# Kernel tuning notes

Hardware: AMD Instinct MI355X
Metric: run time of the kernel (lower is better)

## Reference

```python
import jax, jax.numpy as jnp
import numpy as np

EMBED = 512
WINDOW = 64

def setup_inputs() -> dict:
    key = jax.random.key(0)
    ks = jax.random.split(key, 5)
    B, S, E = 4, 4096, EMBED
    s = 1.0 / np.sqrt(E)
    x = jax.random.normal(ks[0], (B, S, E), dtype=jnp.float32)
    W_qkv = jax.random.uniform(ks[1], (E, 3 * E), minval=-s, maxval=s, dtype=jnp.float32)
    b_qkv = jax.random.uniform(ks[2], (3 * E,), minval=-s, maxval=s, dtype=jnp.float32)
    W_out = jax.random.uniform(ks[3], (E, E), minval=-s, maxval=s, dtype=jnp.float32)
    b_out = jax.random.uniform(ks[4], (E,), minval=-s, maxval=s, dtype=jnp.float32)
    return {"x": x, "W_qkv": W_qkv, "b_qkv": b_qkv, "W_out": W_out, "b_out": b_out}

def reference(x, W_qkv, b_qkv, W_out, b_out):
    B, S, E = x.shape
    scale = jnp.sqrt(jnp.asarray(E, dtype=x.dtype))
    qkv = x @ W_qkv + b_qkv                    # [B,S,3E]
    q, k, v = jnp.split(qkv, 3, axis=-1)       # each [B,S,E]
    scores = jnp.einsum('bqe,bke->bqk', q, k) / scale  # [B,S,S]
    pos = jnp.arange(S)
    dist = pos[None, :] - pos[:, None]         # [S,S]
    window_mask = jnp.abs(dist) <= WINDOW
    neg_inf = jnp.asarray(-jnp.inf, dtype=scores.dtype)
    scores = jnp.where(window_mask[None, :, :], scores, neg_inf)
    attn = jax.nn.softmax(scores, axis=-1)     # every row has in-window entries
    attended = jnp.einsum('bqk,bke->bqe', attn, v)
    return attended @ W_out + b_out
```

## Files before the change

### kernel.cpp

```cpp
#include <hip/hip_runtime.h>

typedef __attribute__((ext_vector_type(8))) _Float16 f16x8;
typedef __attribute__((ext_vector_type(4))) _Float16 f16x4;
typedef __attribute__((ext_vector_type(4))) float f32x4;
typedef __attribute__((address_space(1))) const char gc_char;
typedef __attribute__((address_space(3))) char ls_char;

#define MFMA(a, b, c) __builtin_amdgcn_mfma_f32_16x16x32_f16((a), (b), (c), 0, 0, 0)
#define FENCE() asm volatile("" ::: "memory")
#define BARRIER() do { FENCE(); __builtin_amdgcn_s_barrier(); FENCE(); } while (0)
#define VMW(n) asm volatile("s_waitcnt vmcnt(" #n ")" ::: "memory")

static constexpr int SEQ = 4096;
static constexpr int EMB = 512;
static constexpr float QSCALE = 0.04419417382415922f;

__device__ __forceinline__ void gl_lds16(const void* g, void* l) {
    __builtin_amdgcn_global_load_lds((gc_char*)g, (ls_char*)l, 16, 0, 0);
}

__global__ void k_prep(const float* __restrict__ x, _Float16* __restrict__ xb,
                       const float* __restrict__ Wq, _Float16* __restrict__ WqT,
                       const float* __restrict__ Wo, _Float16* __restrict__ WoT) {
    const int bid = blockIdx.x, tid = threadIdx.x;
    if (bid < 4096) {
        long i = (long)bid * 256 + tid;
        const float4* p = (const float4*)x + i * 2;
        float4 a = p[0], b = p[1];
        f16x8 v;
        v[0] = (_Float16)a.x; v[1] = (_Float16)a.y; v[2] = (_Float16)a.z; v[3] = (_Float16)a.w;
        v[4] = (_Float16)b.x; v[5] = (_Float16)b.y; v[6] = (_Float16)b.z; v[7] = (_Float16)b.w;
        *(f16x8*)(xb + i * 8) = v;
    } else {
        __shared__ float Ls[64][65];
        int t = bid - 4096;
        const float* W; _Float16* WT; int N, k0, n0;
        if (t < 192) { W = Wq; WT = WqT; N = 1536; k0 = (t & 7) * 64; n0 = (t >> 3) * 64; }
        else { t -= 192; W = Wo; WT = WoT; N = 512; k0 = (t & 7) * 64; n0 = (t >> 3) * 64; }
        int c = tid & 63, r4 = tid >> 6;
#pragma unroll
        for (int i = 0; i < 16; ++i) {
            int row = i * 4 + r4;
            Ls[row][c] = W[(long)(k0 + row) * N + n0 + c];
        }
        __syncthreads();
#pragma unroll
        for (int i = 0; i < 16; ++i) {
            int row = i * 4 + r4;
            WT[(long)(n0 + row) * 512 + k0 + c] = (_Float16)Ls[c][row];
        }
    }
}

__launch_bounds__(512, 1) __global__
void k_gemm_qkv(const _Float16* __restrict__ A, const _Float16* __restrict__ BT,
                const float* __restrict__ bias,
                _Float16* __restrict__ Qo, _Float16* __restrict__ Ko, _Float16* __restrict__ VT) {
    extern __shared__ __align__(16) char smem[];
    const int tid = threadIdx.x, lane = tid & 63, w = tid >> 6, g = lane >> 4, f = lane & 15;
    const int wrow = w >> 2, wcol = w & 3;
    const int bid = blockIdx.x;
    const int swz = (bid & 7) * 96 + (bid >> 3);
    const int brow = swz / 6, bcol = swz - brow * 6;
    const long row0 = (long)brow * 128;
    const int col0 = bcol * 256;
    const char* Abase = (const char*)A + row0 * 1024;
    const char* Bbase = (const char*)BT + (long)col0 * 1024;

    f32x4 acc[4][4] = {};
    f16x8 a[2][2], breg[2][2][2];

    auto stageA = [&](int h, char* dst, int kt) {
        int rr = tid >> 3;
        int ch = (tid & 7) ^ (rr & 7);
        int grow = h * 32 + (rr & 31) + (rr >> 5) * 64;
        gl_lds16(Abase + (long)grow * 1024 + kt * 128 + ch * 16, dst + h * 8192 + tid * 16);
    };
    auto stageB = [&](int h, char* dst, int kt) {
#pragma unroll
        for (int it = 0; it < 2; ++it) {
            int s = it * 512 + tid;
            int cc = s >> 3;
            int ch = (s & 7) ^ (cc & 7);
            int gcol = h * 32 + (cc & 31) + (cc >> 5) * 64;
            gl_lds16(Bbase + (long)gcol * 1024 + kt * 128 + ch * 16,
                     dst + 16384 + h * 16384 + s * 16);
        }
    };
    auto ldA = [&](const char* buf, int mh) {
#pragma unroll
        for (int mi = 0; mi < 2; ++mi)
#pragma unroll
            for (int ks = 0; ks < 2; ++ks) {
                int rr = wrow * 32 + mi * 16 + f;
                int cl = ks * 4 + g;
                a[mi][ks] = *(const f16x8*)(buf + mh * 8192 + rr * 128 + ((cl ^ (rr & 7)) << 4));
            }
    };
    auto ldB = [&](const char* buf, int nh) {
#pragma unroll
        for (int ni = 0; ni < 2; ++ni)
#pragma unroll
            for (int ks = 0; ks < 2; ++ks) {
                int cc = wcol * 32 + ni * 16 + f;
                int cl = ks * 4 + g;
                breg[nh][ni][ks] =
                    *(const f16x8*)(buf + 16384 + nh * 16384 + cc * 128 + ((cl ^ (cc & 7)) << 4));
            }
    };
    auto mfma8 = [&](int mh, int nh) {
        __builtin_amdgcn_s_setprio(1);
#pragma unroll
        for (int mi = 0; mi < 2; ++mi)
#pragma unroll
            for (int ni = 0; ni < 2; ++ni)
#pragma unroll
                for (int ks = 0; ks < 2; ++ks)
                    acc[mh * 2 + mi][nh * 2 + ni] =
                        MFMA(a[mi][ks], breg[nh][ni][ks], acc[mh * 2 + mi][nh * 2 + ni]);
        __builtin_amdgcn_s_setprio(0);
    };

    stageB(0, smem, 0);
    stageA(0, smem, 0); stageA(1, smem, 0);
    stageB(1, smem, 0);
    VMW(3);
    BARRIER();

    for (int kt = 0; kt < 8; ++kt) {
        const char* cur = smem + (kt & 1) * 49152;
        char* nxt = smem + ((kt + 1) & 1) * 49152;
        const bool last = (kt == 7);
        ldA(cur, 0); ldB(cur, 0);
        if (!last) stageB(0, nxt, kt + 1);
        BARRIER();
        mfma8(0, 0);
        if (!last) { VMW(2); } else { VMW(0); }
        BARRIER();
        ldB(cur, 1);
        if (!last) { stageA(0, nxt, kt + 1); stageA(1, nxt, kt + 1); }
        BARRIER();
        mfma8(0, 1);
        BARRIER();
        ldA(cur, 1);
        if (!last) stageB(1, nxt, kt + 1);
        BARRIER();
        mfma8(1, 0);
        BARRIER();
        mfma8(1, 1);
        if (!last) { VMW(3); }
        BARRIER();
    }

    float bv[4];
#pragma unroll
    for (int ni = 0; ni < 4; ++ni) bv[ni] = bias[col0 + wcol * 64 + ni * 16 + f];

    if (col0 >= 1024) {
#pragma unroll
        for (int mi = 0; mi < 4; ++mi)
#pragma unroll
            for (int ni = 0; ni < 4; ++ni) {
                int r0 = wrow * 64 + mi * 16 + g * 4;
                int c = wcol * 64 + ni * 16 + f;
                f16x4 v4;
#pragma unroll
                for (int j = 0; j < 4; ++j) v4[j] = (_Float16)(acc[mi][ni][j] + bv[ni]);
                *(f16x4*)(smem + c * 256 + ((r0 * 2) ^ ((c & 7) << 4))) = v4;
            }
        __syncthreads();
        int bb = (int)(row0 >> 12);
        _Float16* vt = VT + ((long)bb * 512 + (col0 - 1024)) * 4096 + (row0 & 4095);
#pragma unroll
        for (int it = 0; it < 8; ++it) {
            int slot = it * 512 + tid;
            int e = slot >> 4, ch = slot & 15;
            f16x8 v = *(const f16x8*)(smem + e * 256 + ((ch * 16) ^ ((e & 7) << 4)));
            *(f16x8*)(vt + (long)e * 4096 + ch * 8) = v;
        }
    } else {
        const float sc = (col0 < 512) ? QSCALE : 1.0f;
#pragma unroll
        for (int mi = 0; mi < 4; ++mi)
#pragma unroll
            for (int ni = 0; ni < 4; ++ni)
#pragma unroll
                for (int j = 0; j < 4; ++j) {
                    int r = wrow * 64 + mi * 16 + g * 4 + j;
                    int c = wcol * 64 + ni * 16 + f;
                    float v = (acc[mi][ni][j] + bv[ni]) * sc;
                    int pc = ((c >> 3) + ((r >> 2) & 7) * 2) & 31;
                    *(_Float16*)(smem + r * 512 + pc * 16 + (c & 7) * 2) = (_Float16)v;
                }
        __syncthreads();
        _Float16* dst = (col0 < 512) ? Qo : Ko;
        int cofs = (col0 < 512) ? col0 : col0 - 512;
#pragma unroll
        for (int it = 0; it < 8; ++it) {
            int slot = it * 512 + tid;
            int r = slot >> 5, ch = slot & 31;
            int pc = (ch + ((r >> 2) & 7) * 2) & 31;
            f16x8 v = *(const f16x8*)(smem + r * 512 + pc * 16);
            *(f16x8*)(dst + (row0 + r) * 512 + cofs + ch * 8) = v;
        }
    }
}

__launch_bounds__(512, 1) __global__
void k_attn(const _Float16* __restrict__ Qb, const _Float16* __restrict__ Kb,
            const _Float16* __restrict__ VT, const _Float16* __restrict__ WoT,
            const float* __restrict__ bout, float* __restrict__ Out) {
    extern __shared__ __align__(16) char smem[];
    char* buf[2] = { smem, smem + 49152 };
    char* Pl = smem + 98304;
    float* Mp = (float*)(smem + 123904);
    float* Lp = (float*)(smem + 124928);

    const int tid = threadIdx.x, w = tid >> 6, lane = tid & 63, g = lane >> 4, f = lane & 15;
    const int rh = w >> 2, kh = w & 3;
    const int bid = blockIdx.x;
    const int swzb = (bid & 7) * 32 + (bid >> 3);
    const int b = swzb >> 6, qt = swzb & 63;
    const int q0 = qt * 64, kbase = q0 - 64;
    const long bofs = (long)b * SEQ;

    f16x8 qf[2][16];
#pragma unroll
    for (int mt = 0; mt < 2; ++mt) {
        const _Float16* qr = Qb + (bofs + q0 + rh * 32 + mt * 16 + f) * EMB + g * 8;
#pragma unroll
        for (int ks = 0; ks < 16; ++ks) qf[mt][ks] = *(const f16x8*)(qr + ks * 32);
    }

    auto stageK = [&](int ec, char* dst) {
#pragma unroll
        for (int it = 0; it < 6; ++it) {
            int slot = it * 512 + tid;
            int r = slot >> 4, c = slot & 15;
            int cs = c ^ (r & 7);
            int key = min(max(kbase + r, 0), SEQ - 1);
            gl_lds16(Kb + (bofs + key) * EMB + ec * 128 + cs * 8, dst + slot * 16);
        }
    };
    auto stageVT = [&](int ec, char* dst) {
#pragma unroll
        for (int it = 0; it < 6; ++it) {
            int slot = it * 512 + tid;
            int r = slot / 24, c = slot - r * 24;
            int cs = c ^ (r & 7);
            int k0 = min(max(kbase + cs * 8, 0), SEQ - 8);
            gl_lds16(VT + ((long)b * 512 + ec * 128 + r) * 4096 + k0, dst + slot * 16);
        }
    };

    f32x4 sacc[2][3] = {};
    stageK(0, buf[0]);
    for (int ec = 0; ec < 4; ++ec) {
        if (ec < 3) stageK(ec + 1, buf[(ec + 1) & 1]);
        else stageVT(0, buf[0]);
        VMW(6);
        BARRIER();
        const char* kb = buf[ec & 1];
#pragma unroll
        for (int kk = 0; kk < 4; ++kk) {
#pragma unroll
            for (int t = 0; t < 3; ++t) {
                int n = kh * 48 + t * 16 + f;
                f16x8 bf = *(const f16x8*)(kb + n * 256 + (((kk * 4 + g) ^ (n & 7)) << 4));
#pragma unroll
                for (int mt = 0; mt < 2; ++mt)
                    sacc[mt][t] = MFMA(qf[mt][ec * 4 + kk], bf, sacc[mt][t]);
            }
        }
        BARRIER();
    }

    float m[2][4] = {{-3e30f, -3e30f, -3e30f, -3e30f}, {-3e30f, -3e30f, -3e30f, -3e30f}};
    float l[2][4] = {};
#pragma unroll
    for (int mt = 0; mt < 2; ++mt)
#pragma unroll
        for (int t = 0; t < 3; ++t) {
            int key = kbase + kh * 48 + t * 16 + f;
            bool kv = (key >= 0) && (key < SEQ);
#pragma unroll
            for (int j = 0; j < 4; ++j) {
                int d = key - (q0 + rh * 32 + mt * 16 + g * 4 + j);
                bool valid = kv && (d >= -64) && (d <= 64);
                float s = valid ? sacc[mt][t][j] : -3e30f;
                sacc[mt][t][j] = s;
                m[mt][j] = fmaxf(m[mt][j], s);
            }
        }
#pragma unroll
    for (int mt = 0; mt < 2; ++mt)
#pragma unroll
        for (int j = 0; j < 4; ++j) {
            m[mt][j] = fmaxf(m[mt][j], __shfl_xor(m[mt][j], 1));
            m[mt][j] = fmaxf(m[mt][j], __shfl_xor(m[mt][j], 2));
            m[mt][j] = fmaxf(m[mt][j], __shfl_xor(m[mt][j], 4));
            m[mt][j] = fmaxf(m[mt][j], __shfl_xor(m[mt][j], 8));
        }
    if (f == 0) {
#pragma unroll
        for (int mt = 0; mt < 2; ++mt)
#pragma unroll
            for (int j = 0; j < 4; ++j)
                Mp[kh * 64 + rh * 32 + mt * 16 + g * 4 + j] = m[mt][j];
    }
    __syncthreads();
#pragma unroll
    for (int mt = 0; mt < 2; ++mt)
#pragma unroll
        for (int j = 0; j < 4; ++j) {
            int r = rh * 32 + mt * 16 + g * 4 + j;
            m[mt][j] = fmaxf(fmaxf(Mp[r], Mp[64 + r]), fmaxf(Mp[128 + r], Mp[192 + r]));
        }
#pragma unroll
    for (int mt = 0; mt < 2; ++mt)
#pragma unroll
        for (int t = 0; t < 3; ++t)
#pragma unroll
            for (int j = 0; j < 4; ++j) {
                float p = __expf(sacc[mt][t][j] - m[mt][j]);
                sacc[mt][t][j] = p;
                l[mt][j] += p;
            }
#pragma unroll
    for (int mt = 0; mt < 2; ++mt)
#pragma unroll
        for (int j = 0; j < 4; ++j) {
            l[mt][j] += __shfl_xor(l[mt][j], 1);
            l[mt][j] += __shfl_xor(l[mt][j], 2);
            l[mt][j] += __shfl_xor(l[mt][j], 4);
            l[mt][j] += __shfl_xor(l[mt][j], 8);
        }
    if (f == 0) {
#pragma unroll
        for (int mt = 0; mt < 2; ++mt)
#pragma unroll
            for (int j = 0; j < 4; ++j)
                Lp[kh * 64 + rh * 32 + mt * 16 + g * 4 + j] = l[mt][j];
    }
#pragma unroll
    for (int mt = 0; mt < 2; ++mt)
#pragma unroll
        for (int t = 0; t < 3; ++t)
#pragma unroll
            for (int j = 0; j < 4; ++j)
                *(_Float16*)(Pl + (rh * 32 + mt * 16 + g * 4 + j) * 400 +
                             (kh * 48 + t * 16 + f) * 2) = (_Float16)sacc[mt][t][j];
    __syncthreads();

    float rl[2][4];
#pragma unroll
    for (int mt = 0; mt < 2; ++mt)
#pragma unroll
        for (int j = 0; j < 4; ++j) {
            int r = rh * 32 + mt * 16 + g * 4 + j;
            rl[mt][j] = 1.0f / (Lp[r] + Lp[64 + r] + Lp[128 + r] + Lp[192 + r]);
        }

    f16x8 pf[2][6];
#pragma unroll
    for (int mt = 0; mt < 2; ++mt)
#pragma unroll
        for (int kc = 0; kc < 6; ++kc)
            pf[mt][kc] = *(const f16x8*)(Pl + (rh * 32 + mt * 16 + f) * 400 + kc * 64 + g * 16);

    f32x4 oacc[4][2][2] = {};
    for (int ec = 0; ec < 4; ++ec) {
        if (ec < 3) stageVT(ec + 1, buf[(ec + 1) & 1]);
        if (ec > 0) { if (ec < 3) { VMW(6); } else { VMW(0); } }
        BARRIER();
        const char* vb = buf[ec & 1];
#pragma unroll
        for (int kc = 0; kc < 6; ++kc) {
#pragma unroll
            for (int nt = 0; nt < 2; ++nt) {
                int e = kh * 32 + nt * 16 + f;
                f16x8 vf = *(const f16x8*)(vb + e * 384 + (((kc * 4 + g) ^ (e & 7)) << 4));
#pragma unroll
                for (int mt = 0; mt < 2; ++mt)
                    oacc[ec][mt][nt] = MFMA(pf[mt][kc], vf, oacc[ec][mt][nt]);
            }
        }
        BARRIER();
    }

    __syncthreads();
    char* att = smem;
    char* wb0 = smem + 65536;
    char* wb1 = smem + 98304;

    auto stageW = [&](int u, char* dst) {
#pragma unroll
        for (int i = 0; i < 4; ++i) {
            int s = i * 512 + tid;
            int col = s >> 2, ch = s & 3;
            int gd = (ch - (col >> 1)) & 3;
            gl_lds16(WoT + (long)col * 512 + u * 32 + gd * 8, dst + s * 16);
        }
    };
    stageW(0, wb0);
    stageW(1, wb1);
#pragma unroll
    for (int ec = 0; ec < 4; ++ec)
#pragma unroll
        for (int mt = 0; mt < 2; ++mt)
#pragma unroll
            for (int nt = 0; nt < 2; ++nt)
#pragma unroll
                for (int j = 0; j < 4; ++j) {
                    int row = rh * 32 + mt * 16 + g * 4 + j;
                    int col = ec * 128 + kh * 32 + nt * 16 + f;
                    *(_Float16*)(att + row * 1024 + ((col * 2) ^ ((row & 7) << 4))) =
                        (_Float16)(oacc[ec][mt][nt][j] * rl[mt][j]);
                }
    __syncthreads();

    float bv2[8];
#pragma unroll
    for (int nt = 0; nt < 8; ++nt) bv2[nt] = bout[kh * 128 + nt * 16 + f];

    f32x4 acc2[2][8] = {};
    for (int u = 0; u < 16; ++u) {
        const char* wcur = (u & 1) ? wb1 : wb0;
        f16x8 a2[2];
#pragma unroll
        for (int mt = 0; mt < 2; ++mt) {
            int row = rh * 32 + mt * 16 + f;
            a2[mt] = *(const f16x8*)(att + row * 1024 + ((u * 64 + g * 16) ^ ((row & 7) << 4)));
        }
        __builtin_amdgcn_s_setprio(1);
#pragma unroll
        for (int nt = 0; nt < 8; ++nt) {
            int col = kh * 128 + nt * 16 + f;
            f16x8 b2 = *(const f16x8*)(wcur + col * 64 + (((g + (col >> 1)) & 3) << 4));
#pragma unroll
            for (int mt = 0; mt < 2; ++mt)
                acc2[mt][nt] = MFMA(a2[mt], b2, acc2[mt][nt]);
        }
        __builtin_amdgcn_s_setprio(0);
        BARRIER();
        if (u + 2 < 16) {
            stageW(u + 2, (u & 1) ? wb1 : wb0);
            VMW(4);
        } else {
            VMW(0);
        }
        BARRIER();
    }

#pragma unroll
    for (int mt = 0; mt < 2; ++mt)
#pragma unroll
        for (int nt = 0; nt < 8; ++nt) {
            long r0 = bofs + q0 + rh * 32 + mt * 16 + g * 4;
            int c = kh * 128 + nt * 16 + f;
#pragma unroll
            for (int j = 0; j < 4; ++j)
                Out[(r0 + j) * 512 + c] = acc2[mt][nt][j] + bv2[nt];
        }
}

extern "C" void kernel_launch(void* const* d_in, const int* in_sizes, int n_in,
                              void* d_out, int out_size, void* d_ws, size_t ws_size,
                              hipStream_t stream) {
    const float* x     = (const float*)d_in[0];
    const float* W_qkv = (const float*)d_in[1];
    const float* b_qkv = (const float*)d_in[2];
    const float* W_out = (const float*)d_in[3];
    const float* b_out = (const float*)d_in[4];

    char* ws = (char*)d_ws;
    _Float16* xb    = (_Float16*)(ws);
    _Float16* WqkvT = (_Float16*)(ws + 16777216);
    _Float16* WoutT = (_Float16*)(ws + 16777216 + 1572864);
    _Float16* Qb    = (_Float16*)(ws + 18874368);
    _Float16* Kb    = (_Float16*)(ws + 18874368 + 16777216);
    _Float16* VT    = (_Float16*)(ws + 18874368 + 33554432);
    float* out = (float*)d_out;

    (void)hipFuncSetAttribute((const void*)k_gemm_qkv,
                              hipFuncAttributeMaxDynamicSharedMemorySize, 98304);
    (void)hipFuncSetAttribute((const void*)k_attn,
                              hipFuncAttributeMaxDynamicSharedMemorySize, 131072);

    k_prep<<<4352, 256, 0, stream>>>(x, xb, W_qkv, WqkvT, W_out, WoutT);
    k_gemm_qkv<<<768, 512, 98304, stream>>>(xb, WqkvT, b_qkv, Qb, Kb, VT);
    k_attn<<<256, 512, 131072, stream>>>(Qb, Kb, VT, WoutT, b_out, out);
}
```

Before: 79.89 us.

## Restructure QKV GEMM to 256x256 tiles with 4 waves and 2 blocks per CU

The QKV projection GEMM moves from 128x256 tiles with 8 waves to 256x256 tiles with 4 waves, each wave computing a 128x128 sub-tile with an 8x8 accumulator array. K steps shrink to 32 elements with a simple double-buffered LDS pipeline and one barrier per step, replacing the hand-interleaved multi-barrier schedule. LDS use drops to 64 KB so two blocks can share a CU. The epilogue writes in two halves through LDS. The aim is more data reuse per wave and fewer barriers, at the cost of heavy register pressure (256 accumulator VGPRs) and fewer blocks (384) across the CUs.

```diff
diff --git a/kernel.cpp b/kernel.cpp
--- a/kernel.cpp
+++ b/kernel.cpp
@@ -52,156 +52,129 @@
     }
 }
 
-__launch_bounds__(512, 1) __global__
+__launch_bounds__(256, 2) __global__
 void k_gemm_qkv(const _Float16* __restrict__ A, const _Float16* __restrict__ BT,
                 const float* __restrict__ bias,
                 _Float16* __restrict__ Qo, _Float16* __restrict__ Ko, _Float16* __restrict__ VT) {
     extern __shared__ __align__(16) char smem[];
     const int tid = threadIdx.x, lane = tid & 63, w = tid >> 6, g = lane >> 4, f = lane & 15;
-    const int wrow = w >> 2, wcol = w & 3;
+    const int wr = w >> 1, wc = w & 1;
     const int bid = blockIdx.x;
-    const int swz = (bid & 7) * 96 + (bid >> 3);
+    const int swz = (bid & 7) * 48 + (bid >> 3);
     const int brow = swz / 6, bcol = swz - brow * 6;
-    const long row0 = (long)brow * 128;
+    const long row0 = (long)brow * 256;
     const int col0 = bcol * 256;
     const char* Abase = (const char*)A + row0 * 1024;
     const char* Bbase = (const char*)BT + (long)col0 * 1024;
 
-    f32x4 acc[4][4] = {};
-    f16x8 a[2][2], breg[2][2][2];
-
-    auto stageA = [&](int h, char* dst, int kt) {
-        int rr = tid >> 3;
-        int ch = (tid & 7) ^ (rr & 7);
-        int grow = h * 32 + (rr & 31) + (rr >> 5) * 64;
-        gl_lds16(Abase + (long)grow * 1024 + kt * 128 + ch * 16, dst + h * 8192 + tid * 16);
+    f32x4 acc[8][8] = {};
+
+    auto stage = [&](char* dst, int kt) {
+#pragma unroll
+        for (int it = 0; it < 4; ++it) {
+            int s = it * 256 + tid;
+            int row = s >> 2, ch = s & 3;
+            int gd = ch ^ ((row >> 1) & 3);
+            gl_lds16(Abase + (long)row * 1024 + kt * 64 + gd * 16, dst + s * 16);
+        }
+#pragma unroll
+        for (int it = 0; it < 4; ++it) {
+            int s = it * 256 + tid;
+            int row = s >> 2, ch = s & 3;
+            int gd = ch ^ ((row >> 1) & 3);
+            gl_lds16(Bbase + (long)row * 1024 + kt * 64 + gd * 16, dst + 16384 + s * 16);
+        }
     };
-    auto stageB = [&](int h, char* dst, int kt) {
-#pragma unroll
-        for (int it = 0; it < 2; ++it) {
-            int s = it * 512 + tid;
-            int cc = s >> 3;
-            int ch = (s & 7) ^ (cc & 7);
-            int gcol = h * 32 + (cc & 31) + (cc >> 5) * 64;
-            gl_lds16(Bbase + (long)gcol * 1024 + kt * 128 + ch * 16,
-                     dst + 16384 + h * 16384 + s * 16);
-        }
-    };
-    auto ldA = [&](const char* buf, int mh) {
-#pragma unroll
-        for (int mi = 0; mi < 2; ++mi)
-#pragma unroll
-            for (int ks = 0; ks < 2; ++ks) {
-                int rr = wrow * 32 + mi * 16 + f;
-                int cl = ks * 4 + g;
-                a[mi][ks] = *(const f16x8*)(buf + mh * 8192 + rr * 128 + ((cl ^ (rr & 7)) << 4));
-            }
-    };
-    auto ldB = [&](const char* buf, int nh) {
-#pragma unroll
-        for (int ni = 0; ni < 2; ++ni)
-#pragma unroll
-            for (int ks = 0; ks < 2; ++ks) {
-                int cc = wcol * 32 + ni * 16 + f;
-                int cl = ks * 4 + g;
-                breg[nh][ni][ks] =
-                    *(const f16x8*)(buf + 16384 + nh * 16384 + cc * 128 + ((cl ^ (cc & 7)) << 4));
-            }
-    };
-    auto mfma8 = [&](int mh, int nh) {
+
+    stage(smem, 0);
+
+    for (int kt = 0; kt < 16; ++kt) {
+        const char* cur = smem + (kt & 1) * 32768;
+        char* nxt = smem + ((kt + 1) & 1) * 32768;
+        if (kt < 15) { stage(nxt, kt + 1); VMW(8); } else { VMW(0); }
+        BARRIER();
+        f16x8 a[8], b[8];
+#pragma unroll
+        for (int mi = 0; mi < 8; ++mi) {
+            int rr = wr * 128 + mi * 16 + f;
+            a[mi] = *(const f16x8*)(cur + rr * 64 + ((g ^ ((rr >> 1) & 3)) << 4));
+        }
+#pragma unroll
+        for (int ni = 0; ni < 8; ++ni) {
+            int cc = wc * 128 + ni * 16 + f;
+            b[ni] = *(const f16x8*)(cur + 16384 + cc * 64 + ((g ^ ((cc >> 1) & 3)) << 4));
+        }
         __builtin_amdgcn_s_setprio(1);
 #pragma unroll
-        for (int mi = 0; mi < 2; ++mi)
-#pragma unroll
-            for (int ni = 0; ni < 2; ++ni)
-#pragma unroll
-                for (int ks = 0; ks < 2; ++ks)
-                    acc[mh * 2 + mi][nh * 2 + ni] =
-                        MFMA(a[mi][ks], breg[nh][ni][ks], acc[mh * 2 + mi][nh * 2 + ni]);
+        for (int mi = 0; mi < 8; ++mi)
+#pragma unroll
+            for (int ni = 0; ni < 8; ++ni)
+                acc[mi][ni] = MFMA(a[mi], b[ni], acc[mi][ni]);
         __builtin_amdgcn_s_setprio(0);
-    };
-
-    stageB(0, smem, 0);
-    stageA(0, smem, 0); stageA(1, smem, 0);
-    stageB(1, smem, 0);
-    VMW(3);
-    BARRIER();
-
-    for (int kt = 0; kt < 8; ++kt) {
-        const char* cur = smem + (kt & 1) * 49152;
-        char* nxt = smem + ((kt + 1) & 1) * 49152;
-        const bool last = (kt == 7);
-        ldA(cur, 0); ldB(cur, 0);
-        if (!last) stageB(0, nxt, kt + 1);
-        BARRIER();
-        mfma8(0, 0);
-        if (!last) { VMW(2); } else { VMW(0); }
-        BARRIER();
-        ldB(cur, 1);
-        if (!last) { stageA(0, nxt, kt + 1); stageA(1, nxt, kt + 1); }
-        BARRIER();
-        mfma8(0, 1);
-        BARRIER();
-        ldA(cur, 1);
-        if (!last) stageB(1, nxt, kt + 1);
-        BARRIER();
-        mfma8(1, 0);
-        BARRIER();
-        mfma8(1, 1);
-        if (!last) { VMW(3); }
-        BARRIER();
-    }
-
-    float bv[4];
-#pragma unroll
-    for (int ni = 0; ni < 4; ++ni) bv[ni] = bias[col0 + wcol * 64 + ni * 16 + f];
+        BARRIER();
+    }
+
+    float bv[8];
+#pragma unroll
+    for (int ni = 0; ni < 8; ++ni) bv[ni] = bias[col0 + wc * 128 + ni * 16 + f];
 
     if (col0 >= 1024) {
-#pragma unroll
-        for (int mi = 0; mi < 4; ++mi)
-#pragma unroll
-            for (int ni = 0; ni < 4; ++ni) {
-                int r0 = wrow * 64 + mi * 16 + g * 4;
-                int c = wcol * 64 + ni * 16 + f;
-                f16x4 v4;
-#pragma unroll
-                for (int j = 0; j < 4; ++j) v4[j] = (_Float16)(acc[mi][ni][j] + bv[ni]);
-                *(f16x4*)(smem + c * 256 + ((r0 * 2) ^ ((c & 7) << 4))) = v4;
-            }
-        __syncthreads();
-        int bb = (int)(row0 >> 12);
-        _Float16* vt = VT + ((long)bb * 512 + (col0 - 1024)) * 4096 + (row0 & 4095);
-#pragma unroll
-        for (int it = 0; it < 8; ++it) {
-            int slot = it * 512 + tid;
-            int e = slot >> 4, ch = slot & 15;
-            f16x8 v = *(const f16x8*)(smem + e * 256 + ((ch * 16) ^ ((e & 7) << 4)));
-            *(f16x8*)(vt + (long)e * 4096 + ch * 8) = v;
+        _Float16* vt = VT + ((long)(row0 >> 12) * 512 + (col0 - 1024)) * 4096 + (row0 & 4095);
+#pragma unroll
+        for (int p = 0; p < 2; ++p) {
+            if (p) BARRIER();
+            if (wr == p) {
+#pragma unroll
+                for (int mi = 0; mi < 8; ++mi)
+#pragma unroll
+                    for (int ni = 0; ni < 8; ++ni) {
+                        int k0l = mi * 16 + g * 4;
+                        int e = wc * 128 + ni * 16 + f;
+                        f16x4 v4;
+#pragma unroll
+                        for (int j = 0; j < 4; ++j) v4[j] = (_Float16)(acc[mi][ni][j] + bv[ni]);
+                        *(f16x4*)(smem + e * 256 + ((k0l * 2) ^ ((e & 7) << 4))) = v4;
+                    }
+            }
+            BARRIER();
+#pragma unroll
+            for (int it = 0; it < 16; ++it) {
+                int slot = it * 256 + tid;
+                int e = slot >> 4, ch = slot & 15;
+                f16x8 v = *(const f16x8*)(smem + e * 256 + ((ch * 16) ^ ((e & 7) << 4)));
+                *(f16x8*)(vt + (long)e * 4096 + p * 128 + ch * 8) = v;
+            }
         }
     } else {
         const float sc = (col0 < 512) ? QSCALE : 1.0f;
-#pragma unroll
-        for (int mi = 0; mi < 4; ++mi)
-#pragma unroll
-            for (int ni = 0; ni < 4; ++ni)
-#pragma unroll
-                for (int j = 0; j < 4; ++j) {
-                    int r = wrow * 64 + mi * 16 + g * 4 + j;
-                    int c = wcol * 64 + ni * 16 + f;
-                    float v = (acc[mi][ni][j] + bv[ni]) * sc;
-                    int pc = ((c >> 3) + ((r >> 2) & 7) * 2) & 31;
-                    *(_Float16*)(smem + r * 512 + pc * 16 + (c & 7) * 2) = (_Float16)v;
-                }
-        __syncthreads();
         _Float16* dst = (col0 < 512) ? Qo : Ko;
         int cofs = (col0 < 512) ? col0 : col0 - 512;
 #pragma unroll
-        for (int it = 0; it < 8; ++it) {
-            int slot = it * 512 + tid;
-            int r = slot >> 5, ch = slot & 31;
-            int pc = (ch + ((r >> 2) & 7) * 2) & 31;
-            f16x8 v = *(const f16x8*)(smem + r * 512 + pc * 16);
-            *(f16x8*)(dst + (row0 + r) * 512 + cofs + ch * 8) = v;
+        for (int p = 0; p < 2; ++p) {
+            if (p) BARRIER();
+            if (wr == p) {
+#pragma unroll
+                for (int mi = 0; mi < 8; ++mi)
+#pragma unroll
+                    for (int ni = 0; ni < 8; ++ni)
+#pragma unroll
+                        for (int j = 0; j < 4; ++j) {
+                            int r = mi * 16 + g * 4 + j;
+                            int c = wc * 128 + ni * 16 + f;
+                            float v = (acc[mi][ni][j] + bv[ni]) * sc;
+                            int pc = ((c >> 3) + ((r >> 2) & 7) * 2) & 31;
+                            *(_Float16*)(smem + r * 512 + pc * 16 + (c & 7) * 2) = (_Float16)v;
+                        }
+            }
+            BARRIER();
+#pragma unroll
+            for (int it = 0; it < 16; ++it) {
+                int slot = it * 256 + tid;
+                int r = slot >> 5, ch = slot & 31;
+                int pc = (ch + ((r >> 2) & 7) * 2) & 31;
+                f16x8 v = *(const f16x8*)(smem + r * 512 + pc * 16);
+                *(f16x8*)(dst + (row0 + p * 128 + r) * 512 + cofs + ch * 8) = v;
+            }
         }
     }
 }
@@ -483,11 +456,11 @@
     float* out = (float*)d_out;
 
     (void)hipFuncSetAttribute((const void*)k_gemm_qkv,
-                              hipFuncAttributeMaxDynamicSharedMemorySize, 98304);
+                              hipFuncAttributeMaxDynamicSharedMemorySize, 65536);
     (void)hipFuncSetAttribute((const void*)k_attn,
                               hipFuncAttributeMaxDynamicSharedMemorySize, 131072);
 
     k_prep<<<4352, 256, 0, stream>>>(x, xb, W_qkv, WqkvT, W_out, WoutT);
-    k_gemm_qkv<<<768, 512, 98304, stream>>>(xb, WqkvT, b_qkv, Qb, Kb, VT);
+    k_gemm_qkv<<<384, 256, 65536, stream>>>(xb, WqkvT, b_qkv, Qb, Kb, VT);
     k_attn<<<256, 512, 131072, stream>>>(Qb, Kb, VT, WoutT, b_out, out);
 }
```

New measurement: 252.2 us. 216% more time.
